# Kernel optimization log

Hardware: AMD Instinct MI355X
Metric: run time of the kernel (lower is better)

The kernel has to match this reference:

```python
import jax, jax.numpy as jnp
import numpy as np

N_NODES = 50000
N_EDGES = 800000
IN_C, HID_C, OUT_C = 128, 128, 64


def setup_inputs() -> dict:
    key = jax.random.key(0)
    ks = jax.random.split(key, 8)
    x = jax.random.normal(ks[0], (N_NODES, IN_C), dtype=jnp.float32)
    edge_index = jax.random.randint(ks[1], (2, N_EDGES), 0, N_NODES, dtype=jnp.int64)
    s = 1.0 / np.sqrt(IN_C)
    W1_l = jax.random.uniform(ks[2], (HID_C, IN_C), jnp.float32, -s, s)
    W1_r = jax.random.uniform(ks[3], (HID_C, IN_C), jnp.float32, -s, s)
    b1 = jnp.zeros((HID_C,), jnp.float32)
    s2 = 1.0 / np.sqrt(HID_C)
    W2_l = jax.random.uniform(ks[4], (OUT_C, HID_C), jnp.float32, -s2, s2)
    W2_r = jax.random.uniform(ks[5], (OUT_C, HID_C), jnp.float32, -s2, s2)
    b2 = jnp.zeros((OUT_C,), jnp.float32)
    return {"x": x, "edge_index": edge_index, "W1_l": W1_l, "W1_r": W1_r,
            "b1": b1, "W2_l": W2_l, "W2_r": W2_r, "b2": b2}


def _sage_conv(x, src, dst, W_l, W_r, b, n_nodes):
    # mean aggregation of source-node features onto target nodes
    agg = jax.ops.segment_sum(x[src], dst, num_segments=n_nodes)  # [N, d]
    deg = jax.ops.segment_sum(jnp.ones((src.shape[0],), x.dtype), dst,
                              num_segments=n_nodes)               # [N]
    agg = agg / jnp.maximum(deg, 1.0)[:, None]
    # out = lin_l(agg) + lin_r(x) + bias (PyG SAGEConv, root_weight=True)
    return agg @ W_l.T + x @ W_r.T + b


def reference(x, edge_index, W1_l, W1_r, b1, W2_l, W2_r, b2):
    src, dst = edge_index[0], edge_index[1]
    n = x.shape[0]
    h = _sage_conv(x, src, dst, W1_l, W1_r, b1, n)
    h = jax.nn.relu(h)
    # dropout is identity in eval mode (training=False)
    out = _sage_conv(h, src, dst, W2_l, W2_r, b2, n)
    return jax.nn.log_softmax(out, axis=1)
```

## Files before the change

kernel.cpp:

```cpp
#include <hip/hip_runtime.h>
#include <hip/hip_bf16.h>

#define IN_C  128
#define HID_C 128
#define OUT_C 64
#define PAD   48
#define EPB   4096
#define CAP   40
#define MAX_NBUCK 512

typedef __attribute__((ext_vector_type(8))) short short8;
typedef __attribute__((ext_vector_type(4))) float f32x4;

__device__ __forceinline__ unsigned short f2bf(float f) {
  unsigned int u = __float_as_uint(f);
  unsigned int r = (u + 0x7fffu + ((u >> 16) & 1u)) >> 16;
  return (unsigned short)r;
}
__device__ __forceinline__ float bflo(unsigned int v) { return __uint_as_float(v << 16); }
__device__ __forceinline__ float bfhi(unsigned int v) { return __uint_as_float(v & 0xffff0000u); }
__device__ __forceinline__ float bf2f(unsigned short u) { return __uint_as_float((unsigned int)u << 16); }

__global__ __launch_bounds__(256) void k_bucket3(
    const int* __restrict__ src, const int* __restrict__ dst,
    const float* __restrict__ X,
    const float* __restrict__ W1l, const float* __restrict__ W1r,
    const float* __restrict__ W2l, const float* __restrict__ W2r,
    unsigned short* __restrict__ ccnt,
    unsigned int* __restrict__ bkts,
    unsigned short* __restrict__ Xb,
    unsigned short* __restrict__ Wb1, unsigned short* __restrict__ Wb2,
    int nE, int nb, int n4, int nbk)
{
  __shared__ int cur[MAX_NBUCK];
  const int blk = blockIdx.x;
  if (blk < nbk) {
    for (int i = threadIdx.x; i < nb; i += 256) cur[i] = 0;
    __syncthreads();
    const int e0 = blk * EPB;
    const int e1 = min(e0 + EPB, nE);
    for (int e = e0 + threadIdx.x; e < e1; e += 256) {
      int d = dst[e];
      int b = d >> 7;
      int p = atomicAdd(&cur[b], 1);
      if (p < CAP)
        bkts[((size_t)blk * nb + b) * CAP + p] =
            ((unsigned int)(d & 127) << 16) | (unsigned int)src[e];
    }
    __syncthreads();
    for (int i = threadIdx.x; i < nb; i += 256)
      ccnt[(size_t)blk * nb + i] = (unsigned short)cur[i];
    return;
  }
  int i = (blk - nbk) * 256 + threadIdx.x;
  if (i < n4) {
    float4 v = ((const float4*)X)[i];
    uint2 o;
    o.x = (unsigned int)f2bf(v.x) | ((unsigned int)f2bf(v.y) << 16);
    o.y = (unsigned int)f2bf(v.z) | ((unsigned int)f2bf(v.w) << 16);
    ((uint2*)Xb)[i] = o;
    return;
  }
  int j = i - n4;
  if (j < 128 * 256) {
    int o = j >> 8, k = j & 255;
    float v = (k < 128) ? W1l[o * 128 + k] : W1r[o * 128 + (k - 128)];
    Wb1[j] = f2bf(v);
    return;
  }
  int k2 = j - 128 * 256;
  if (k2 < 128 * 128) {
    int o = k2 >> 7, k = k2 & 127;
    float v = (o < 64) ? W2l[o * 128 + k] : W2r[(o - 64) * 128 + k];
    Wb2[k2] = f2bf(v);
  }
}

__global__ __launch_bounds__(256) void k_csr2(const unsigned int* __restrict__ bkts,
                                              const unsigned short* __restrict__ ccnt,
                                              int* __restrict__ cnt,
                                              unsigned short* __restrict__ csr,
                                              int n, int nbk, int nb) {
  __shared__ int lc[128];
  __shared__ unsigned short lcsr[128 * PAD];
  const int b = blockIdx.x;
  const int base = b << 7;
  const int lim = min(128, n - base);
  for (int i = threadIdx.x; i < 128; i += 256) lc[i] = 0;
  __syncthreads();
  for (int j = threadIdx.x; j < nbk; j += 256) {
    int mj = min((int)ccnt[(size_t)j * nb + b], CAP);
    const unsigned int* cell = bkts + ((size_t)j * nb + b) * CAP;
    for (int i = 0; i < mj; ++i) {
      unsigned int p = cell[i];
      int d = p >> 16;
      int pos = atomicAdd(&lc[d], 1);
      if (pos < PAD) lcsr[d * PAD + pos] = (unsigned short)(p & 0xffffu);
    }
  }
  __syncthreads();
  for (int i = threadIdx.x; i < lim; i += 256) cnt[base + i] = min(lc[i], PAD) | (lc[i] << 8);
  uint4* co = (uint4*)(csr + (size_t)base * PAD);
  const uint4* ci = (const uint4*)lcsr;
  const int nu = lim * 6;
  for (int i = threadIdx.x; i < nu; i += 256) co[i] = ci[i];
}

__global__ __launch_bounds__(256) void k_gather(const unsigned short* __restrict__ Xb,
                                                const int* __restrict__ cnt,
                                                const unsigned short* __restrict__ csr,
                                                unsigned short* __restrict__ aggb, int n) {
  const int lane = threadIdx.x & 63;
  const int node = blockIdx.x * 4 + __builtin_amdgcn_readfirstlane(threadIdx.x >> 6);
  if (node >= n) return;
  const int c = cnt[node];
  const int deg = c >> 8;
  const int m = c & 255;
  const short8* rwv = (const short8*)(csr + (size_t)node * PAD);
  const unsigned int* Xp = (const unsigned int*)Xb;
  float ax = 0.0f, ay = 0.0f;

#define G1_GROUP(g)                                                          \
  if ((g) * 8 < m) {                                                         \
    short8 I = rwv[g];                                                       \
    unsigned int v[8];                                                       \
    _Pragma("unroll") for (int t = 0; t < 8; ++t) {                          \
      int s = ((g) * 8 + t < m) ? (int)(unsigned short)I[t] : 0;             \
      v[t] = Xp[(size_t)s * 64 + lane];                                      \
    }                                                                        \
    _Pragma("unroll") for (int t = 0; t < 8; ++t)                            \
      if ((g) * 8 + t < m) { ax += bflo(v[t]); ay += bfhi(v[t]); }           \
  }
  G1_GROUP(0) G1_GROUP(1) G1_GROUP(2) G1_GROUP(3) G1_GROUP(4) G1_GROUP(5)
#undef G1_GROUP

  const float invd = 1.0f / fmaxf((float)deg, 1.0f);
  unsigned int o = (unsigned int)f2bf(ax * invd) | ((unsigned int)f2bf(ay * invd) << 16);
  ((unsigned int*)aggb)[(size_t)node * 64 + lane] = o;
}

__global__ __launch_bounds__(512) void k_gemm1(
    const unsigned short* __restrict__ aggb, const unsigned short* __restrict__ xb,
    const unsigned short* __restrict__ Wb,
    const float* __restrict__ bias,
    unsigned short* __restrict__ hb, int nRows)
{
  __shared__ unsigned short wlds[128 * 256];

  const int lane = threadIdx.x & 63;
  const int w = threadIdx.x >> 6;
  const int lr = lane & 15;
  const int kg = lane >> 4;
  const int sw = lr & 7;
  const int r0 = blockIdx.x * 128 + w * 16;
  int arow = r0 + lr;
  if (arow >= nRows) arow = nRows - 1;

  short8 aA[4], aX[4];
#pragma unroll
  for (int kc = 0; kc < 4; ++kc) {
    aA[kc] = *(const short8*)(aggb + (size_t)arow * 128 + kc * 32 + kg * 8);
    aX[kc] = *(const short8*)(xb   + (size_t)arow * 128 + kc * 32 + kg * 8);
  }

  {
    const uint4* gw = (const uint4*)Wb;
    uint4* lw = (uint4*)wlds;
#pragma unroll
    for (int t = 0; t < 8; ++t) {
      int i = threadIdx.x + t * 512;
      int row = i >> 5, c = i & 31;
      lw[(row << 5) | (c ^ (row & 7))] = gw[i];
    }
  }
  __syncthreads();

  f32x4 acc[8];
#pragma unroll
  for (int ct = 0; ct < 8; ++ct) acc[ct] = (f32x4)(0.0f);

#pragma unroll
  for (int ct = 0; ct < 8; ++ct) {
    const unsigned short* wrowp = wlds + ((ct * 16 + lr) << 8);
#pragma unroll
    for (int kc = 0; kc < 4; ++kc) {
      short8 b0 = *(const short8*)(wrowp + ((((kc * 4 + kg) ^ sw)) << 3));
      acc[ct] = __builtin_amdgcn_mfma_f32_16x16x32_bf16(aA[kc], b0, acc[ct], 0, 0, 0);
    }
#pragma unroll
    for (int kc = 0; kc < 4; ++kc) {
      short8 b1 = *(const short8*)(wrowp + (((16 + ((kc * 4 + kg) ^ sw))) << 3));
      acc[ct] = __builtin_amdgcn_mfma_f32_16x16x32_bf16(aX[kc], b1, acc[ct], 0, 0, 0);
    }
  }

#pragma unroll
  for (int ct = 0; ct < 8; ++ct) {
    const int col = ct * 16 + lr;
    const float b = bias[col];
#pragma unroll
    for (int v = 0; v < 4; ++v) {
      int row = r0 + kg * 4 + v;
      if (row < nRows) {
        float o = fmaxf(acc[ct][v] + b, 0.0f);
        hb[(size_t)row * 128 + col] = f2bf(o);
      }
    }
  }
}

__global__ __launch_bounds__(512) void k_gemm2t(
    const unsigned short* __restrict__ hb,
    const unsigned short* __restrict__ Wb,
    unsigned short* __restrict__ pq, int nRows)
{
  __shared__ unsigned short wlds[128 * 128];

  const int lane = threadIdx.x & 63;
  const int w = threadIdx.x >> 6;
  const int lr = lane & 15;
  const int kg = lane >> 4;
  const int sw = lr & 7;
  const int r0 = blockIdx.x * 128 + w * 16;
  int arow = r0 + lr;
  if (arow >= nRows) arow = nRows - 1;

  short8 aH[4];
#pragma unroll
  for (int kc = 0; kc < 4; ++kc)
    aH[kc] = *(const short8*)(hb + (size_t)arow * 128 + kc * 32 + kg * 8);

  {
    const uint4* gw = (const uint4*)Wb;
    uint4* lw = (uint4*)wlds;
#pragma unroll
    for (int t = 0; t < 4; ++t) {
      int i = threadIdx.x + t * 512;
      int row = i >> 4, c = i & 15;
      lw[(row << 4) | (c ^ (row & 7))] = gw[i];
    }
  }
  __syncthreads();

  f32x4 acc[8];
#pragma unroll
  for (int ct = 0; ct < 8; ++ct) acc[ct] = (f32x4)(0.0f);

#pragma unroll
  for (int ct = 0; ct < 8; ++ct) {
    const unsigned short* wrowp = wlds + ((ct * 16 + lr) << 7);
#pragma unroll
    for (int kc = 0; kc < 4; ++kc) {
      short8 b0 = *(const short8*)(wrowp + ((((kc * 4 + kg) ^ sw)) << 3));
      acc[ct] = __builtin_amdgcn_mfma_f32_16x16x32_bf16(aH[kc], b0, acc[ct], 0, 0, 0);
    }
  }

#pragma unroll
  for (int ct = 0; ct < 8; ++ct) {
    const int col = ct * 16 + lr;
#pragma unroll
    for (int v = 0; v < 4; ++v) {
      int row = r0 + kg * 4 + v;
      if (row < nRows)
        pq[(size_t)row * 128 + col] = f2bf(acc[ct][v]);
    }
  }
}

__global__ __launch_bounds__(256) void k_gather2sm(const unsigned short* __restrict__ pq,
                                                   const int* __restrict__ cnt,
                                                   const unsigned short* __restrict__ csr,
                                                   const float* __restrict__ bias,
                                                   float* __restrict__ OUT, int n) {
  const int lane = threadIdx.x & 63;
  const int node = blockIdx.x * 4 + __builtin_amdgcn_readfirstlane(threadIdx.x >> 6);
  if (node >= n) return;
  const int c = cnt[node];
  const int deg = c >> 8;
  const int m = c & 255;
  const short8* rwv = (const short8*)(csr + (size_t)node * PAD);

  float a = 0.0f;
#define G2_GROUP(g)                                                          \
  if ((g) * 8 < m) {                                                         \
    short8 I = rwv[g];                                                       \
    float v[8];                                                              \
    _Pragma("unroll") for (int t = 0; t < 8; ++t) {                          \
      int s = ((g) * 8 + t < m) ? (int)(unsigned short)I[t] : 0;             \
      v[t] = bf2f(pq[(size_t)s * 128 + lane]);                               \
    }                                                                        \
    _Pragma("unroll") for (int t = 0; t < 8; ++t)                            \
      if ((g) * 8 + t < m) a += v[t];                                        \
  }
  G2_GROUP(0) G2_GROUP(1) G2_GROUP(2) G2_GROUP(3) G2_GROUP(4) G2_GROUP(5)
#undef G2_GROUP

  a *= 1.0f / fmaxf((float)deg, 1.0f);
  float v = a + bf2f(pq[(size_t)node * 128 + 64 + lane]) + bias[lane];

  float mx = v;
#pragma unroll
  for (int mask = 1; mask < 64; mask <<= 1) mx = fmaxf(mx, __shfl_xor(mx, mask));
  float s = __expf(v - mx);
#pragma unroll
  for (int mask = 1; mask < 64; mask <<= 1) s += __shfl_xor(s, mask);
  OUT[(size_t)node * 64 + lane] = v - mx - __logf(s);
}

extern "C" void kernel_launch(void* const* d_in, const int* in_sizes, int n_in,
                              void* d_out, int out_size, void* d_ws, size_t ws_size,
                              hipStream_t stream) {
  const float* x   = (const float*)d_in[0];
  const int*   ei  = (const int*)d_in[1];
  const float* W1l = (const float*)d_in[2];
  const float* W1r = (const float*)d_in[3];
  const float* b1  = (const float*)d_in[4];
  const float* W2l = (const float*)d_in[5];
  const float* W2r = (const float*)d_in[6];
  const float* b2  = (const float*)d_in[7];
  float* out = (float*)d_out;

  const int N  = in_sizes[0] / IN_C;
  const int nE = in_sizes[1] / 2;
  const int* src = ei;
  const int* dst = ei + nE;

  const int nb  = (N + 127) >> 7;
  const int nPad = nb << 7;
  const int nbk = (nE + EPB - 1) / EPB;

  char* w = (char*)d_ws;
  size_t off = 0;
  int* cnt             = (int*)(w + off); off += ((size_t)nPad * 4 + 255) & ~255ull;
  unsigned short* ccnt = (unsigned short*)(w + off); off += ((size_t)nbk * nb * 2 + 255) & ~255ull;
  unsigned int* bkts   = (unsigned int*)(w + off); off += (size_t)nbk * nb * CAP * 4;
  unsigned short* csr  = (unsigned short*)(w + off); off += ((size_t)nPad * PAD * 2 + 255) & ~255ull;
  unsigned short* xb   = (unsigned short*)(w + off); off += (size_t)N * 128 * 2;
  unsigned short* hb   = (unsigned short*)(w + off); off += (size_t)N * 128 * 2;
  unsigned short* aggb = (unsigned short*)(w + off); off += (size_t)N * 128 * 2;
  unsigned short* Wb1  = (unsigned short*)(w + off); off += 128 * 256 * 2;
  unsigned short* Wb2  = (unsigned short*)(w + off); off += 128 * 128 * 2;
  unsigned short* pq   = aggb;

  const int n4 = N * 128 / 4;
  const int prep_items = n4 + 128 * 256 + 128 * 128;
  const int grid_b3 = nbk + (prep_items + 255) / 256;

  k_bucket3<<<grid_b3, 256, 0, stream>>>(src, dst, x, W1l, W1r, W2l, W2r,
                                         ccnt, bkts, xb, Wb1, Wb2, nE, nb, n4, nbk);

  k_csr2<<<nb, 256, 0, stream>>>(bkts, ccnt, cnt, csr, N, nbk, nb);

  k_gather<<<(N + 3) / 4, 256, 0, stream>>>(xb, cnt, csr, aggb, N);
  k_gemm1<<<(N + 127) / 128, 512, 0, stream>>>(aggb, xb, Wb1, b1, hb, N);

  k_gemm2t<<<(N + 127) / 128, 512, 0, stream>>>(hb, Wb2, pq, N);
  k_gather2sm<<<(N + 3) / 4, 256, 0, stream>>>(pq, cnt, csr, b2, out, N);
}
```

Measured before the change: 110.3 us.

## Fuse CSR construction with first-layer neighbor gather in one kernel

Merges the CSR-building kernel and the first mean-aggregation gather into one 1024-thread kernel per 128-node bucket. The gather reads neighbor indices and counts directly from shared memory instead of re-reading them from global memory, and one launch is removed. The trade-off is fewer, larger blocks (about 391), each doing a serial 8-node loop per wave after the bucket scan. That may lower occupancy and latency hiding for the random row gathers compared with the previous fine-grained launch.

```diff
diff --git a/kernel.cpp b/kernel.cpp
--- a/kernel.cpp
+++ b/kernel.cpp
@@ -76,19 +76,25 @@
   }
 }
 
-__global__ __launch_bounds__(256) void k_csr2(const unsigned int* __restrict__ bkts,
-                                              const unsigned short* __restrict__ ccnt,
-                                              int* __restrict__ cnt,
-                                              unsigned short* __restrict__ csr,
-                                              int n, int nbk, int nb) {
+__global__ __launch_bounds__(1024) void k_csrgather(
+    const unsigned int* __restrict__ bkts,
+    const unsigned short* __restrict__ ccnt,
+    const unsigned short* __restrict__ Xb,
+    int* __restrict__ cnt,
+    unsigned short* __restrict__ csr,
+    unsigned short* __restrict__ aggb,
+    int n, int nbk, int nb)
+{
   __shared__ int lc[128];
   __shared__ unsigned short lcsr[128 * PAD];
   const int b = blockIdx.x;
   const int base = b << 7;
   const int lim = min(128, n - base);
-  for (int i = threadIdx.x; i < 128; i += 256) lc[i] = 0;
+  const int tid = threadIdx.x;
+
+  if (tid < 128) lc[tid] = 0;
   __syncthreads();
-  for (int j = threadIdx.x; j < nbk; j += 256) {
+  for (int j = tid; j < nbk; j += 1024) {
     int mj = min((int)ccnt[(size_t)j * nb + b], CAP);
     const unsigned int* cell = bkts + ((size_t)j * nb + b) * CAP;
     for (int i = 0; i < mj; ++i) {
@@ -99,44 +105,45 @@
     }
   }
   __syncthreads();
-  for (int i = threadIdx.x; i < lim; i += 256) cnt[base + i] = min(lc[i], PAD) | (lc[i] << 8);
-  uint4* co = (uint4*)(csr + (size_t)base * PAD);
-  const uint4* ci = (const uint4*)lcsr;
-  const int nu = lim * 6;
-  for (int i = threadIdx.x; i < nu; i += 256) co[i] = ci[i];
-}
-
-__global__ __launch_bounds__(256) void k_gather(const unsigned short* __restrict__ Xb,
-                                                const int* __restrict__ cnt,
-                                                const unsigned short* __restrict__ csr,
-                                                unsigned short* __restrict__ aggb, int n) {
-  const int lane = threadIdx.x & 63;
-  const int node = blockIdx.x * 4 + __builtin_amdgcn_readfirstlane(threadIdx.x >> 6);
-  if (node >= n) return;
-  const int c = cnt[node];
-  const int deg = c >> 8;
-  const int m = c & 255;
-  const short8* rwv = (const short8*)(csr + (size_t)node * PAD);
+
+  if (tid < lim) cnt[base + tid] = min(lc[tid], PAD) | (lc[tid] << 8);
+  {
+    uint4* co = (uint4*)(csr + (size_t)base * PAD);
+    const uint4* ci = (const uint4*)lcsr;
+    const int nu = lim * 6;
+    for (int i = tid; i < nu; i += 1024) co[i] = ci[i];
+  }
+
+  const int lane = tid & 63;
+  const int wv = tid >> 6;
   const unsigned int* Xp = (const unsigned int*)Xb;
-  float ax = 0.0f, ay = 0.0f;
+#pragma unroll 1
+  for (int it = 0; it < 8; ++it) {
+    const int nl = wv * 8 + it;
+    if (nl >= lim) break;
+    const int rawc = lc[nl];
+    const int m = min(rawc, PAD);
+    const short8* rwv = (const short8*)(lcsr + nl * PAD);
+    float ax = 0.0f, ay = 0.0f;
 
 #define G1_GROUP(g)                                                          \
-  if ((g) * 8 < m) {                                                         \
-    short8 I = rwv[g];                                                       \
-    unsigned int v[8];                                                       \
-    _Pragma("unroll") for (int t = 0; t < 8; ++t) {                          \
-      int s = ((g) * 8 + t < m) ? (int)(unsigned short)I[t] : 0;             \
-      v[t] = Xp[(size_t)s * 64 + lane];                                      \
-    }                                                                        \
-    _Pragma("unroll") for (int t = 0; t < 8; ++t)                            \
-      if ((g) * 8 + t < m) { ax += bflo(v[t]); ay += bfhi(v[t]); }           \
-  }
-  G1_GROUP(0) G1_GROUP(1) G1_GROUP(2) G1_GROUP(3) G1_GROUP(4) G1_GROUP(5)
+    if ((g) * 8 < m) {                                                       \
+      short8 I = rwv[g];                                                     \
+      unsigned int v[8];                                                     \
+      _Pragma("unroll") for (int t = 0; t < 8; ++t) {                        \
+        int s = ((g) * 8 + t < m) ? (int)(unsigned short)I[t] : 0;           \
+        v[t] = Xp[(size_t)s * 64 + lane];                                    \
+      }                                                                      \
+      _Pragma("unroll") for (int t = 0; t < 8; ++t)                          \
+        if ((g) * 8 + t < m) { ax += bflo(v[t]); ay += bfhi(v[t]); }         \
+    }
+    G1_GROUP(0) G1_GROUP(1) G1_GROUP(2) G1_GROUP(3) G1_GROUP(4) G1_GROUP(5)
 #undef G1_GROUP
 
-  const float invd = 1.0f / fmaxf((float)deg, 1.0f);
-  unsigned int o = (unsigned int)f2bf(ax * invd) | ((unsigned int)f2bf(ay * invd) << 16);
-  ((unsigned int*)aggb)[(size_t)node * 64 + lane] = o;
+    const float invd = 1.0f / fmaxf((float)rawc, 1.0f);
+    unsigned int o = (unsigned int)f2bf(ax * invd) | ((unsigned int)f2bf(ay * invd) << 16);
+    ((unsigned int*)aggb)[(size_t)(base + nl) * 64 + lane] = o;
+  }
 }
 
 __global__ __launch_bounds__(512) void k_gemm1(
@@ -350,9 +357,8 @@
   k_bucket3<<<grid_b3, 256, 0, stream>>>(src, dst, x, W1l, W1r, W2l, W2r,
                                          ccnt, bkts, xb, Wb1, Wb2, nE, nb, n4, nbk);
 
-  k_csr2<<<nb, 256, 0, stream>>>(bkts, ccnt, cnt, csr, N, nbk, nb);
-
-  k_gather<<<(N + 3) / 4, 256, 0, stream>>>(xb, cnt, csr, aggb, N);
+  k_csrgather<<<nb, 1024, 0, stream>>>(bkts, ccnt, xb, cnt, csr, aggb, N, nbk, nb);
+
   k_gemm1<<<(N + 127) / 128, 512, 0, stream>>>(aggb, xb, Wb1, b1, hb, N);
 
   k_gemm2t<<<(N + 127) / 128, 512, 0, stream>>>(hb, Wb2, pq, N);
```

Result: no change. 108.9 us (-1.2%).
